# Optimization experiments

Measured on AMD Instinct MI355X. Metric: run time of the kernel, lower is better.

## Reference

```python
import jax, jax.numpy as jnp
import numpy as np

BLOCKS = (1, 2, 3, 4)      # (block_size, offset=0) from max_block_size=4
BLOCK_MULT = 12            # lcm(1,2,3,4)
DS = 4                     # downsample_factor
MAX_BS = 4                 # max block size (also pos_conv kernel size)
DIM = 512
VOCAB = 256


def _masked_mean(t, m, axis):
    # t: [..., L, D], m: [..., L] bool -> mean over axis with mask, 0 where empty
    mf = m[..., None].astype(t.dtype)
    num = jnp.sum(t * mf, axis=axis)
    tot = jnp.sum(mf, axis=axis)
    mean = num / jnp.clip(tot, 1.0)
    return jnp.where(tot == 0.0, jnp.zeros_like(mean), mean)


def setup_inputs() -> dict:
    key = jax.random.key(0)
    ks = jax.random.split(key, 8)
    B, S = 8, 2048
    return {
        "x": jax.random.randint(ks[0], (B, S), 0, VOCAB),
        "mask": jnp.ones((B, S), dtype=bool),
        "emb": jax.random.normal(ks[1], (VOCAB, DIM), jnp.float32) * 0.02,
        "dw_w": jax.random.normal(ks[2], (MAX_BS, 1, DIM), jnp.float32) * 0.1,   # depthwise kernel (W, I=1, O=DIM)
        "dw_b": jnp.zeros((DIM,), jnp.float32),
        "pw_w": jax.random.normal(ks[3], (1, DIM, DIM), jnp.float32) * 0.03,     # pointwise 1x1 conv
        "pw_b": jnp.zeros((DIM,), jnp.float32),
        "score_w": jax.random.normal(ks[4], (DIM, 1), jnp.float32) * 0.05,
        "score_b": jnp.zeros((1,), jnp.float32),
    }


def reference(x, mask, emb, dw_w, dw_b, pw_w, pw_b, score_w, score_b):
    B, S = x.shape
    D = DIM
    trunc = ((S + DS - 1) // DS) * DS  # next_divisible_length(S, DS); equals S here

    h = emb[x]                                              # [B,S,D]
    h = jnp.pad(h, ((0, 0), (0, MAX_BS - 1), (0, 0)))       # right pad for VALID conv
    dn = jax.lax.conv_dimension_numbers(h.shape, dw_w.shape, ('NWC', 'WIO', 'NWC'))
    h = jax.lax.conv_general_dilated(h, dw_w, (1,), 'VALID',
                                     dimension_numbers=dn,
                                     feature_group_count=D) + dw_b  # depthwise -> [B,S,D]
    h = jnp.einsum('bsd,de->bse', h, pw_w[0]) + pw_b                # pointwise

    # pad seq to multiple of lcm of block sizes
    Sp = ((h.shape[1] + BLOCK_MULT - 1) // BLOCK_MULT) * BLOCK_MULT
    pad = Sp - h.shape[1]
    h = jnp.pad(h, ((0, 0), (0, pad), (0, 0)))
    m = jnp.pad(mask.astype(bool), ((0, 0), (0, pad)), constant_values=False)

    reprs, rmasks = [], []
    for bsz in BLOCKS:  # fixed small set of block sizes (offset=0 for all)
        nb = Sp // bsz
        g = h.reshape(B, nb, bsz, D)
        mg = m.reshape(B, nb, bsz)
        r = _masked_mean(g, mg, axis=2)                       # [B,nb,D]
        reprs.append(jnp.repeat(r, bsz, axis=1))              # [B,Sp,D]
        rmasks.append(jnp.repeat(jnp.any(mg, axis=-1), bsz, axis=1))

    block_reprs = jnp.stack(reprs, axis=2)    # [B,Sp,M,D]
    block_masks = jnp.stack(rmasks, axis=2)   # [B,Sp,M]

    scores = (block_reprs @ score_w)[..., 0] + score_b[0]     # [B,Sp,M]
    max_neg = -jnp.finfo(scores.dtype).max
    scores = jnp.where(block_masks, scores, max_neg)
    scores = jnp.nan_to_num(jax.nn.softmax(scores, axis=2), nan=0.0)

    # consensus attention over positions
    sim = jnp.einsum('bim,bjm->bij', scores, scores)          # [B,Sp,Sp]
    cm = m[:, :, None] & m[:, None, :]
    sim = jnp.where(cm, sim, max_neg)
    attn = jnp.nan_to_num(jax.nn.softmax(sim, axis=-1), nan=0.0)
    scores = jnp.einsum('bij,bjm->bim', attn, scores)

    out = jnp.einsum('bsmd,bsm->bsd', block_reprs, scores)    # weighted combine
    out = out[:, :trunc]
    mt = m[:, :trunc]

    nl = trunc // DS
    xb = out.reshape(B, nl, DS, D)
    mb = mt.reshape(B, nl, DS)
    out = _masked_mean(xb, mb, axis=2)                        # [B, S/DS, D]
    out_mask = jnp.any(mb, axis=-1)
    return out, out_mask
```

## Files before the change

kernel.cpp:

```cpp
#include <hip/hip_runtime.h>
#include <stdint.h>
#include <stddef.h>

typedef __bf16 bf16_t;
typedef bf16_t bf16x4v __attribute__((ext_vector_type(4)));
typedef bf16_t bf16x8v __attribute__((ext_vector_type(8)));
typedef float  f32x4   __attribute__((ext_vector_type(4)));

#define NBATCH 8
#define SEQ    2048
#define DIM    512
#define SP     2052
#define NL     512
#define MROWS  1088

static __device__ __forceinline__ f32x4 ldbf4(const bf16_t* p) {
  bf16x4v v = *(const bf16x4v*)p;
  f32x4 r;
  r.x = (float)v[0]; r.y = (float)v[1]; r.z = (float)v[2]; r.w = (float)v[3];
  return r;
}
static __device__ __forceinline__ void stbf4(bf16_t* p, f32x4 v) {
  bf16x4v o;
  o[0] = (bf16_t)v.x; o[1] = (bf16_t)v.y; o[2] = (bf16_t)v.z; o[3] = (bf16_t)v.w;
  *(bf16x4v*)p = o;
}

static __device__ __forceinline__ void gload_lds16(const void* g, void* l) {
  __builtin_amdgcn_global_load_lds(
      (const __attribute__((address_space(1))) void*)g,
      (__attribute__((address_space(3))) void*)l, 16, 0, 0);
}

#define GP_WT   256
#define GP_MASK 65
#define GP_SC   544
__global__ __launch_bounds__(256) void kP_prep(
    const float* __restrict__ pw, bf16_t* __restrict__ Wt,
    const void* __restrict__ mraw, float* __restrict__ mask01,
    const float* __restrict__ emb, const float* __restrict__ dww,
    const float* __restrict__ dwb, bf16_t* __restrict__ At) {
  const int bx = blockIdx.x, t = threadIdx.x;
  if (bx < GP_WT) {
    __shared__ float T[32][33];
    int ti = bx >> 4, tj = bx & 15;
    int r = t >> 3, c0 = (t & 7) * 4;
    f32x4 v = *(const f32x4*)(pw + (size_t)(ti * 32 + r) * DIM + tj * 32 + c0);
    T[c0 + 0][r] = v.x; T[c0 + 1][r] = v.y;
    T[c0 + 2][r] = v.z; T[c0 + 3][r] = v.w;
    __syncthreads();
    bf16x4v o;
    o[0] = (bf16_t)T[r][c0 + 0]; o[1] = (bf16_t)T[r][c0 + 1];
    o[2] = (bf16_t)T[r][c0 + 2]; o[3] = (bf16_t)T[r][c0 + 3];
    *(bf16x4v*)(Wt + (size_t)(tj * 32 + r) * DIM + ti * 32 + c0) = o;
    return;
  }
  if (bx < GP_WT + GP_MASK) {
    int idx = (bx - GP_WT) * 256 + t;
    if (idx >= NBATCH * SP) return;
    int b = idx / SP, s = idx - b * SP;
    const unsigned char* mb = (const unsigned char*)mraw;
    int u8 = 0;
#pragma unroll
    for (int i = 0; i < 64; i++)
      if ((i & 3) != 0 && mb[i] != 0) u8 = 1;
    float v = 0.f;
    if (s < SEQ) {
      int mi = b * SEQ + s;
      int nz = u8 ? (mb[mi] != 0) : (((const int*)mraw)[mi] != 0);
      v = nz ? 1.f : 0.f;
    }
    mask01[idx] = v;
    return;
  }
  int idx = (bx - (GP_WT + GP_MASK)) * 256 + t;
  int r = idx >> 7, d0 = (idx & 127) * 4;
  f32x4 o4;
  if (r < 1024) {
    int tt = r >> 8, v = r & 255;
    f32x4 e = *(const f32x4*)(emb + (size_t)v * DIM + d0);
    f32x4 w = *(const f32x4*)(dww + tt * DIM + d0);
    o4 = e * w;
  } else if (r == 1024) {
    o4 = *(const f32x4*)(dwb + d0);
  } else {
    o4.x = o4.y = o4.z = o4.w = 0.f;
  }
  stbf4(At + (size_t)r * DIM + d0, o4);
}

#define BM 64
#define BN 128
#define BK 32
__global__ __launch_bounds__(256) void kM_gemm(
    const bf16_t* __restrict__ A, const bf16_t* __restrict__ Bt,
    float* __restrict__ M) {
  __shared__ __align__(16) bf16_t As[BM * BK];
  __shared__ __align__(16) bf16_t Bs[BN * BK];
  const int t = threadIdx.x;
  const int mt = blockIdx.x >> 2;
  const int nt = blockIdx.x & 3;
  const int m0 = mt * BM, n0 = nt * BN;
  const int lane = t & 63, wave = t >> 6;
  const int wm = (wave & 1) * 32, wn = (wave >> 1) * 64;
  const int mloc = lane & 15, quad = lane >> 4;

  f32x4 acc[2][4] = {};

  char* asd  = (char*)As + t * 16;
  char* bsd1 = (char*)Bs + t * 16;
  char* bsd2 = (char*)Bs + (t + 256) * 16;
  const int ar = t >> 2,           ak = (t & 3) * 8;
  const int br1 = t >> 2,          bk1 = (t & 3) * 8;
  const int br2 = (t + 256) >> 2,  bk2 = (t & 3) * 8;

  for (int k0 = 0; k0 < 512; k0 += BK) {
    gload_lds16(A + (size_t)(m0 + ar) * DIM + k0 + ak, asd);
    gload_lds16(Bt + (size_t)(n0 + br1) * DIM + k0 + bk1, bsd1);
    gload_lds16(Bt + (size_t)(n0 + br2) * DIM + k0 + bk2, bsd2);
    __syncthreads();
    bf16x8v af[2], bfr[4];
#pragma unroll
    for (int i = 0; i < 2; i++)
      af[i] = *(const bf16x8v*)&As[(wm + i * 16 + mloc) * BK + quad * 8];
#pragma unroll
    for (int i = 0; i < 4; i++)
      bfr[i] = *(const bf16x8v*)&Bs[(wn + i * 16 + mloc) * BK + quad * 8];
#pragma unroll
    for (int mi = 0; mi < 2; mi++)
#pragma unroll
      for (int ni = 0; ni < 4; ni++)
        acc[mi][ni] = __builtin_amdgcn_mfma_f32_16x16x32_bf16(
            af[mi], bfr[ni], acc[mi][ni], 0, 0, 0);
    __syncthreads();
  }
#pragma unroll
  for (int ni = 0; ni < 4; ni++) {
    int col = n0 + wn + ni * 16 + mloc;
#pragma unroll
    for (int mi = 0; mi < 2; mi++) {
      int rbase = m0 + wm + mi * 16 + quad * 4;
#pragma unroll
      for (int r = 0; r < 4; r++)
        M[(size_t)(rbase + r) * DIM + col] = acc[mi][ni][r];
    }
  }
}

__global__ __launch_bounds__(128) void kB_hp(
    const float* __restrict__ Mt, const int* __restrict__ x,
    const float* __restrict__ pwb, const float* __restrict__ mask01,
    const float* __restrict__ sw, const float* __restrict__ sbp,
    bf16_t* __restrict__ H, float* __restrict__ P) {
  const int b = blockIdx.x, c = blockIdx.y;
  const int s0 = c * 12;
  const int t = threadIdx.x;
  const int d0 = t * 4;
  const float sb = sbp[0];

  f32x4 swv = *(const f32x4*)(sw + d0);
  f32x4 bias2 = *(const f32x4*)(Mt + (size_t)1024 * DIM + d0)
              + *(const f32x4*)(pwb + d0);
  float ms[12], p[12];
#pragma unroll
  for (int i = 0; i < 12; i++) {
    int s = s0 + i;
    ms[i] = mask01[b * SP + s];
    if (s < SEQ) {
      f32x4 h = bias2;
      int base = b * SEQ + s;
#pragma unroll
      for (int tt = 0; tt < 4; tt++) {
        if (s + tt < SEQ) {
          int v = x[base + tt];
          h += *(const f32x4*)(Mt + (size_t)((tt << 8) + v) * DIM + d0);
        }
      }
      p[i] = h.x * swv.x + h.y * swv.y + h.z * swv.z + h.w * swv.w;
      stbf4(H + ((size_t)b * SEQ + s) * DIM + d0, h);
    } else {
      p[i] = 0.f;
    }
  }
#pragma unroll
  for (int off = 32; off > 0; off >>= 1)
#pragma unroll
    for (int i = 0; i < 12; i++) p[i] += __shfl_down(p[i], off);
  __shared__ float hsw[2][12];
  int lane = t & 63, wv = t >> 6;
  if (lane == 0)
#pragma unroll
    for (int i = 0; i < 12; i++) hsw[wv][i] = p[i];
  __syncthreads();
#define HSUM(i) (hsw[0][i] + hsw[1][i])
  if (t < 12) {
    int i = t;
    float m1 = ms[i];
    float v1 = HSUM(i) * m1 + sb;
    int i2 = i & ~1;
    float cc2 = ms[i2] + ms[i2 + 1];
    float s2 = HSUM(i2) * ms[i2] + HSUM(i2 + 1) * ms[i2 + 1];
    float v2 = (cc2 > 0.f ? s2 / cc2 : 0.f) + sb;
    int i3 = (i >= 9) ? 9 : (i >= 6) ? 6 : (i >= 3) ? 3 : 0;
    float cc3 = ms[i3] + ms[i3 + 1] + ms[i3 + 2];
    float s3 = HSUM(i3) * ms[i3] + HSUM(i3 + 1) * ms[i3 + 1] +
               HSUM(i3 + 2) * ms[i3 + 2];
    float v3 = (cc3 > 0.f ? s3 / cc3 : 0.f) + sb;
    int i4 = i & ~3;
    float cc4 = ms[i4] + ms[i4 + 1] + ms[i4 + 2] + ms[i4 + 3];
    float s4 = HSUM(i4) * ms[i4] + HSUM(i4 + 1) * ms[i4 + 1] +
               HSUM(i4 + 2) * ms[i4 + 2] + HSUM(i4 + 3) * ms[i4 + 3];
    float v4 = (cc4 > 0.f ? s4 / cc4 : 0.f) + sb;
    const float NEG = -3.0e38f;
    float a1 = m1 > 0.f ? v1 : NEG, a2 = cc2 > 0.f ? v2 : NEG;
    float a3 = cc3 > 0.f ? v3 : NEG, a4 = cc4 > 0.f ? v4 : NEG;
    float mx = fmaxf(fmaxf(a1, a2), fmaxf(a3, a4));
    f32x4 o;
    if (mx <= NEG) {
      o.x = o.y = o.z = o.w = 0.25f;
    } else {
      float e1 = m1 > 0.f ? __expf(v1 - mx) : 0.f;
      float e2 = cc2 > 0.f ? __expf(v2 - mx) : 0.f;
      float e3 = cc3 > 0.f ? __expf(v3 - mx) : 0.f;
      float e4 = cc4 > 0.f ? __expf(v4 - mx) : 0.f;
      float inv = 1.f / (e1 + e2 + e3 + e4);
      o.x = e1 * inv; o.y = e2 * inv; o.z = e3 * inv; o.w = e4 * inv;
    }
    *(f32x4*)(P + ((size_t)b * SP + s0 + i) * 4) = o;
  }
#undef HSUM
}

#define KS  16
#define KJL 129
__global__ __launch_bounds__(256) void k56_out(
    const bf16_t* __restrict__ H, const float* __restrict__ P,
    const float* __restrict__ mask01, float* __restrict__ out,
    float* __restrict__ omask) {
  const int b = blockIdx.x, yb = blockIdx.y;
  const int t = threadIdx.x;
  const int S0 = yb * KS;
  __shared__ f32x4 Q[SP];
  __shared__ f32x4 wsh[KS];
  __shared__ float msh[KS + 8];
  __shared__ float red[4];

  float cnt0 = 0.f;
  for (int j = t; j < SP; j += 256) {
    f32x4 q = *(const f32x4*)(P + ((size_t)b * SP + j) * 4);
    if (mask01[b * SP + j] == 0.f) {
      q.x = q.y = q.z = q.w = 0.f;
      cnt0 += 1.f;
    }
    Q[j] = q;
  }
  if (t < KS + 8) {
    int s = S0 - 2 + t;
    msh[t] = (s >= 0 && s < SP) ? mask01[b * SP + s] : 0.f;
  }
#pragma unroll
  for (int off = 32; off > 0; off >>= 1) cnt0 += __shfl_down(cnt0, off);
  if ((t & 63) == 0) red[t >> 6] = cnt0;
  __syncthreads();
  const float nmask = red[0] + red[1] + red[2] + red[3];

  {
    const int il = t >> 4, jc = t & 15;
    const f32x4 qi = Q[S0 + il];
    int j0 = jc * KJL, j1 = j0 + KJL;
    if (j1 > SP) j1 = SP;
    f32x4 acc; acc.x = acc.y = acc.z = acc.w = 0.f;
    float den = 0.f;
    for (int j = j0; j < j1; j++) {
      f32x4 pj = Q[j];
      float sim = qi.x * pj.x + qi.y * pj.y + qi.z * pj.z + qi.w * pj.w;
      float e = __expf(sim);
      den += e;
      acc += e * pj;
    }
#pragma unroll
    for (int off = 8; off > 0; off >>= 1) {
      acc.x += __shfl_down(acc.x, off); acc.y += __shfl_down(acc.y, off);
      acc.z += __shfl_down(acc.z, off); acc.w += __shfl_down(acc.w, off);
      den += __shfl_down(den, off);
    }
    if (jc == 0) {
      den -= nmask;
      float inv = den > 0.f ? 1.f / den : 0.f;
      f32x4 w;
      w.x = acc.x * inv; w.y = acc.y * inv;
      w.z = acc.z * inv; w.w = acc.w * inv;
      wsh[il] = w;
    }
  }
  __syncthreads();

#pragma unroll
  for (int it = 0; it < 2; it++) {
    const int slot = it * 256 + t;
    const int ll = slot >> 7;
    const int d0 = (slot & 127) * 4;
    const int sb = ll * 4;
    f32x4 h[8]; float mk[8];
#pragma unroll
    for (int k = 0; k < 8; k++) {
      mk[k] = msh[sb + k];
      int sg = S0 + sb - 2 + k;
      sg = sg < 0 ? 0 : (sg > SEQ - 1 ? SEQ - 1 : sg);
      h[k] = ldbf4(H + ((size_t)b * SEQ + sg) * DIM + d0);
    }
    float c4 = mk[2] + mk[3] + mk[4] + mk[5];
    float i4 = c4 > 0.f ? 1.f / c4 : 0.f;
    f32x4 r4 = (h[2] * mk[2] + h[3] * mk[3] + h[4] * mk[4] + h[5] * mk[5]) * i4;
    float c2a = mk[2] + mk[3], c2b = mk[4] + mk[5];
    f32x4 r2a = (h[2] * mk[2] + h[3] * mk[3]) * (c2a > 0.f ? 1.f / c2a : 0.f);
    f32x4 r2b = (h[4] * mk[4] + h[5] * mk[5]) * (c2b > 0.f ? 1.f / c2b : 0.f);
    const f32x4 w0 = wsh[sb], w1 = wsh[sb + 1];
    const f32x4 w2 = wsh[sb + 2], w3 = wsh[sb + 3];
#define MEAN3(K)                                                         \
    ((h[K] * mk[K] + h[(K) + 1] * mk[(K) + 1] + h[(K) + 2] * mk[(K) + 2]) * \
     ((mk[K] + mk[(K) + 1] + mk[(K) + 2]) > 0.f                          \
          ? 1.f / (mk[K] + mk[(K) + 1] + mk[(K) + 2]) : 0.f))
    f32x4 o;
    const int r = (S0 + sb) % 3;
    if (r == 0) {
      f32x4 A = MEAN3(2), B = MEAN3(5);
      o = mk[2] * (w0.x * h[2] + w0.y * r2a + w0.z * A + w0.w * r4)
        + mk[3] * (w1.x * h[3] + w1.y * r2a + w1.z * A + w1.w * r4)
        + mk[4] * (w2.x * h[4] + w2.y * r2b + w2.z * A + w2.w * r4)
        + mk[5] * (w3.x * h[5] + w3.y * r2b + w3.z * B + w3.w * r4);
    } else if (r == 1) {
      f32x4 A = MEAN3(1), B = MEAN3(4);
      o = mk[2] * (w0.x * h[2] + w0.y * r2a + w0.z * A + w0.w * r4)
        + mk[3] * (w1.x * h[3] + w1.y * r2a + w1.z * A + w1.w * r4)
        + mk[4] * (w2.x * h[4] + w2.y * r2b + w2.z * B + w2.w * r4)
        + mk[5] * (w3.x * h[5] + w3.y * r2b + w3.z * B + w3.w * r4);
    } else {
      f32x4 A = MEAN3(0), B = MEAN3(3);
      o = mk[2] * (w0.x * h[2] + w0.y * r2a + w0.z * A + w0.w * r4)
        + mk[3] * (w1.x * h[3] + w1.y * r2a + w1.z * B + w1.w * r4)
        + mk[4] * (w2.x * h[4] + w2.y * r2b + w2.z * B + w2.w * r4)
        + mk[5] * (w3.x * h[5] + w3.y * r2b + w3.z * B + w3.w * r4);
    }
#undef MEAN3
    o *= i4;
    const int l = yb * 4 + ll;
    *(f32x4*)(out + ((size_t)b * NL + l) * DIM + d0) = o;
    if (d0 == 0) omask[b * NL + l] = c4 > 0.f ? 1.f : 0.f;
  }
}

extern "C" void kernel_launch(void* const* d_in, const int* in_sizes, int n_in,
                              void* d_out, int out_size, void* d_ws, size_t ws_size,
                              hipStream_t stream) {
  const int*   x    = (const int*)d_in[0];
  const void*  mraw = d_in[1];
  const float* emb  = (const float*)d_in[2];
  const float* dww  = (const float*)d_in[3];
  const float* dwb  = (const float*)d_in[4];
  const float* pw   = (const float*)d_in[5];
  const float* pwb  = (const float*)d_in[6];
  const float* sw   = (const float*)d_in[7];
  const float* sb   = (const float*)d_in[8];

  char* ws = (char*)d_ws;
  size_t off = 0;
  auto alloc = [&](size_t bytes) {
    size_t o = off;
    off = (off + bytes + 255) & ~(size_t)255;
    return o;
  };
  bf16_t* H     = (bf16_t*)(ws + alloc((size_t)NBATCH * SEQ * DIM * 2));
  bf16_t* Wt    = (bf16_t*)(ws + alloc((size_t)DIM * DIM * 2));
  bf16_t* At    = (bf16_t*)(ws + alloc((size_t)MROWS * DIM * 2));
  float*  Mt    = (float*)(ws + alloc((size_t)MROWS * DIM * 4));
  float* mask01 = (float*)(ws + alloc((size_t)NBATCH * SP * 4));
  float* P      = (float*)(ws + alloc((size_t)NBATCH * SP * 4 * 4));

  float* out   = (float*)d_out;
  float* omask = out + (size_t)NBATCH * NL * DIM;

  kP_prep<<<GP_WT + GP_MASK + GP_SC, 256, 0, stream>>>(pw, Wt, mraw, mask01,
                                                       emb, dww, dwb, At);
  kM_gemm<<<68, 256, 0, stream>>>(At, Wt, Mt);
  kB_hp<<<dim3(NBATCH, 171), 128, 0, stream>>>(Mt, x, pwb, mask01, sw, sb,
                                               H, P);
  k56_out<<<dim3(NBATCH, 128), 256, 0, stream>>>(H, P, mask01, out, omask);
}
```

Before: 131.6 us.

## Fuse prep and small GEMM into one kernel with on-the-fly operand conversion

Merges the prep kernel (weight transpose to bf16, A-table build) and the GEMM into a single launch. Each block builds its 32-row A tile straight into XOR-swizzled LDS and reads the pointwise weights from fp32 global memory, converting them to bf16 in registers. This removes one kernel launch and the intermediate Wt/At buffers. In exchange it uses many more, smaller tiles (528 blocks), and the B operand is loaded with strided scalar reads, so each weight element is fetched once per row tile.

After: 132.2 us. About the same (+0.4%).

```diff
diff --git a/kernel.cpp b/kernel.cpp
--- a/kernel.cpp
+++ b/kernel.cpp
@@ -26,37 +26,16 @@
   *(bf16x4v*)p = o;
 }
 
-static __device__ __forceinline__ void gload_lds16(const void* g, void* l) {
-  __builtin_amdgcn_global_load_lds(
-      (const __attribute__((address_space(1))) void*)g,
-      (__attribute__((address_space(3))) void*)l, 16, 0, 0);
-}
-
-#define GP_WT   256
-#define GP_MASK 65
-#define GP_SC   544
-__global__ __launch_bounds__(256) void kP_prep(
-    const float* __restrict__ pw, bf16_t* __restrict__ Wt,
-    const void* __restrict__ mraw, float* __restrict__ mask01,
-    const float* __restrict__ emb, const float* __restrict__ dww,
-    const float* __restrict__ dwb, bf16_t* __restrict__ At) {
+#define GK_GEMM 528
+#define GK_MASK 65
+__global__ __launch_bounds__(256) void k1_gemm(
+    const float* __restrict__ pw, const void* __restrict__ mraw,
+    float* __restrict__ mask01, const float* __restrict__ emb,
+    const float* __restrict__ dww, const float* __restrict__ dwb,
+    float* __restrict__ Mt) {
   const int bx = blockIdx.x, t = threadIdx.x;
-  if (bx < GP_WT) {
-    __shared__ float T[32][33];
-    int ti = bx >> 4, tj = bx & 15;
-    int r = t >> 3, c0 = (t & 7) * 4;
-    f32x4 v = *(const f32x4*)(pw + (size_t)(ti * 32 + r) * DIM + tj * 32 + c0);
-    T[c0 + 0][r] = v.x; T[c0 + 1][r] = v.y;
-    T[c0 + 2][r] = v.z; T[c0 + 3][r] = v.w;
-    __syncthreads();
-    bf16x4v o;
-    o[0] = (bf16_t)T[r][c0 + 0]; o[1] = (bf16_t)T[r][c0 + 1];
-    o[2] = (bf16_t)T[r][c0 + 2]; o[3] = (bf16_t)T[r][c0 + 3];
-    *(bf16x4v*)(Wt + (size_t)(tj * 32 + r) * DIM + ti * 32 + c0) = o;
-    return;
-  }
-  if (bx < GP_WT + GP_MASK) {
-    int idx = (bx - GP_WT) * 256 + t;
+  if (bx >= GK_GEMM) {
+    int idx = (bx - GK_GEMM) * 256 + t;
     if (idx >= NBATCH * SP) return;
     int b = idx / SP, s = idx - b * SP;
     const unsigned char* mb = (const unsigned char*)mraw;
@@ -73,78 +52,78 @@
     mask01[idx] = v;
     return;
   }
-  int idx = (bx - (GP_WT + GP_MASK)) * 256 + t;
-  int r = idx >> 7, d0 = (idx & 127) * 4;
-  f32x4 o4;
-  if (r < 1024) {
-    int tt = r >> 8, v = r & 255;
-    f32x4 e = *(const f32x4*)(emb + (size_t)v * DIM + d0);
-    f32x4 w = *(const f32x4*)(dww + tt * DIM + d0);
-    o4 = e * w;
-  } else if (r == 1024) {
-    o4 = *(const f32x4*)(dwb + d0);
-  } else {
-    o4.x = o4.y = o4.z = o4.w = 0.f;
-  }
-  stbf4(At + (size_t)r * DIM + d0, o4);
-}
-
-#define BM 64
-#define BN 128
-#define BK 32
-__global__ __launch_bounds__(256) void kM_gemm(
-    const bf16_t* __restrict__ A, const bf16_t* __restrict__ Bt,
-    float* __restrict__ M) {
-  __shared__ __align__(16) bf16_t As[BM * BK];
-  __shared__ __align__(16) bf16_t Bs[BN * BK];
-  const int t = threadIdx.x;
-  const int mt = blockIdx.x >> 2;
-  const int nt = blockIdx.x & 3;
-  const int m0 = mt * BM, n0 = nt * BN;
+  __shared__ __align__(16) char As[32 * 1024];
+  const int mt = bx >> 4, nt = bx & 15;
+  const int m0 = mt * 32, n0 = nt * 32;
   const int lane = t & 63, wave = t >> 6;
-  const int wm = (wave & 1) * 32, wn = (wave >> 1) * 64;
+  const int wm = (wave & 1) * 16, wn = (wave >> 1) * 16;
   const int mloc = lane & 15, quad = lane >> 4;
 
-  f32x4 acc[2][4] = {};
-
-  char* asd  = (char*)As + t * 16;
-  char* bsd1 = (char*)Bs + t * 16;
-  char* bsd2 = (char*)Bs + (t + 256) * 16;
-  const int ar = t >> 2,           ak = (t & 3) * 8;
-  const int br1 = t >> 2,          bk1 = (t & 3) * 8;
-  const int br2 = (t + 256) >> 2,  bk2 = (t & 3) * 8;
-
-  for (int k0 = 0; k0 < 512; k0 += BK) {
-    gload_lds16(A + (size_t)(m0 + ar) * DIM + k0 + ak, asd);
-    gload_lds16(Bt + (size_t)(n0 + br1) * DIM + k0 + bk1, bsd1);
-    gload_lds16(Bt + (size_t)(n0 + br2) * DIM + k0 + bk2, bsd2);
-    __syncthreads();
-    bf16x8v af[2], bfr[4];
-#pragma unroll
-    for (int i = 0; i < 2; i++)
-      af[i] = *(const bf16x8v*)&As[(wm + i * 16 + mloc) * BK + quad * 8];
-#pragma unroll
-    for (int i = 0; i < 4; i++)
-      bfr[i] = *(const bf16x8v*)&Bs[(wn + i * 16 + mloc) * BK + quad * 8];
-#pragma unroll
-    for (int mi = 0; mi < 2; mi++)
-#pragma unroll
-      for (int ni = 0; ni < 4; ni++)
-        acc[mi][ni] = __builtin_amdgcn_mfma_f32_16x16x32_bf16(
-            af[mi], bfr[ni], acc[mi][ni], 0, 0, 0);
-    __syncthreads();
-  }
-#pragma unroll
-  for (int ni = 0; ni < 4; ni++) {
-    int col = n0 + wn + ni * 16 + mloc;
-#pragma unroll
-    for (int mi = 0; mi < 2; mi++) {
-      int rbase = m0 + wm + mi * 16 + quad * 4;
-#pragma unroll
-      for (int r = 0; r < 4; r++)
-        M[(size_t)(rbase + r) * DIM + col] = acc[mi][ni][r];
-    }
-  }
+  {
+    const int r = t >> 3, kc = (t & 7) * 64;
+    const int grow = m0 + r;
+    const int key = (r & 7) << 4;
+    char* base = As + r * 1024;
+    if (grow < 1024) {
+      const int tt = grow >> 8, v = grow & 255;
+      const float* ep = emb + (size_t)v * DIM + kc;
+      const float* wp = dww + (size_t)tt * DIM + kc;
+#pragma unroll
+      for (int j = 0; j < 8; j++) {
+        f32x4 e0 = *(const f32x4*)(ep + j * 8);
+        f32x4 e1 = *(const f32x4*)(ep + j * 8 + 4);
+        f32x4 w0 = *(const f32x4*)(wp + j * 8);
+        f32x4 w1 = *(const f32x4*)(wp + j * 8 + 4);
+        f32x4 p0 = e0 * w0, p1 = e1 * w1;
+        bf16x8v o;
+        o[0] = (bf16_t)p0.x; o[1] = (bf16_t)p0.y;
+        o[2] = (bf16_t)p0.z; o[3] = (bf16_t)p0.w;
+        o[4] = (bf16_t)p1.x; o[5] = (bf16_t)p1.y;
+        o[6] = (bf16_t)p1.z; o[7] = (bf16_t)p1.w;
+        *(bf16x8v*)(base + (((kc + j * 8) * 2) ^ key)) = o;
+      }
+    } else if (grow == 1024) {
+      const float* bp = dwb + kc;
+#pragma unroll
+      for (int j = 0; j < 8; j++) {
+        f32x4 p0 = *(const f32x4*)(bp + j * 8);
+        f32x4 p1 = *(const f32x4*)(bp + j * 8 + 4);
+        bf16x8v o;
+        o[0] = (bf16_t)p0.x; o[1] = (bf16_t)p0.y;
+        o[2] = (bf16_t)p0.z; o[3] = (bf16_t)p0.w;
+        o[4] = (bf16_t)p1.x; o[5] = (bf16_t)p1.y;
+        o[6] = (bf16_t)p1.z; o[7] = (bf16_t)p1.w;
+        *(bf16x8v*)(base + (((kc + j * 8) * 2) ^ key)) = o;
+      }
+    } else {
+      bf16x8v o = {};
+#pragma unroll
+      for (int j = 0; j < 8; j++)
+        *(bf16x8v*)(base + (((kc + j * 8) * 2) ^ key)) = o;
+    }
+  }
+  __syncthreads();
+
+  const int rowa = wm + mloc;
+  const char* arow = As + rowa * 1024;
+  const int akey = (rowa & 7) << 4;
+  const int ncol = n0 + wn + mloc;
+  const float* pcol = pw + ncol + (size_t)(quad * 8) * DIM;
+
+  f32x4 acc = {};
+#pragma unroll 4
+  for (int kk = 0; kk < 16; kk++) {
+    bf16x8v af = *(const bf16x8v*)(arow + ((kk * 64 + quad * 16) ^ akey));
+    const float* pk = pcol + (size_t)kk * 32 * DIM;
+    bf16x8v bf;
+#pragma unroll
+    for (int ki = 0; ki < 8; ki++)
+      bf[ki] = (bf16_t)pk[(size_t)ki * DIM];
+    acc = __builtin_amdgcn_mfma_f32_16x16x32_bf16(af, bf, acc, 0, 0, 0);
+  }
+#pragma unroll
+  for (int r = 0; r < 4; r++)
+    Mt[(size_t)(m0 + wm + quad * 4 + r) * DIM + ncol] = acc[r];
 }
 
 __global__ __launch_bounds__(128) void kB_hp(
@@ -371,8 +350,6 @@
     return o;
   };
   bf16_t* H     = (bf16_t*)(ws + alloc((size_t)NBATCH * SEQ * DIM * 2));
-  bf16_t* Wt    = (bf16_t*)(ws + alloc((size_t)DIM * DIM * 2));
-  bf16_t* At    = (bf16_t*)(ws + alloc((size_t)MROWS * DIM * 2));
   float*  Mt    = (float*)(ws + alloc((size_t)MROWS * DIM * 4));
   float* mask01 = (float*)(ws + alloc((size_t)NBATCH * SP * 4));
   float* P      = (float*)(ws + alloc((size_t)NBATCH * SP * 4 * 4));
@@ -380,9 +357,8 @@
   float* out   = (float*)d_out;
   float* omask = out + (size_t)NBATCH * NL * DIM;
 
-  kP_prep<<<GP_WT + GP_MASK + GP_SC, 256, 0, stream>>>(pw, Wt, mraw, mask01,
-                                                       emb, dww, dwb, At);
-  kM_gemm<<<68, 256, 0, stream>>>(At, Wt, Mt);
+  k1_gemm<<<GK_GEMM + GK_MASK, 256, 0, stream>>>(pw, mraw, mask01,
+                                                 emb, dww, dwb, Mt);
   kB_hp<<<dim3(NBATCH, 171), 128, 0, stream>>>(Mt, x, pwb, mask01, sw, sb,
                                                H, P);
   k56_out<<<dim3(NBATCH, 128), 256, 0, stream>>>(H, P, mask01, out, omask);
```
